# Optimization experiments

Measured on AMD Instinct MI355X. Metric: run time of the kernel, lower is better.

Reference implementation:

```python
import jax, jax.numpy as jnp
import numpy as np

N = 50000      # nodes
E = 800000     # edges (avg degree 16)
F_IN = 256     # input feature dim
D = 32         # per-head out dim (layer1)
H1 = 8         # layer1 heads
H2 = 1         # layer2 heads
C = 16         # num_classes


def setup_inputs() -> dict:
    key = jax.random.key(0)
    ks = jax.random.split(key, 11)
    s = 0.05  # weight scale
    return {
        "x": jax.random.normal(ks[0], (N, F_IN), dtype=jnp.float32),
        "src": jax.random.randint(ks[1], (E,), 0, N),
        "dst": jax.random.randint(ks[2], (E,), 0, N),
        "W1": jax.random.normal(ks[3], (F_IN, H1 * D), dtype=jnp.float32) * s,
        "al1": jax.random.normal(ks[4], (H1, D), dtype=jnp.float32) * s,
        "ar1": jax.random.normal(ks[5], (H1, D), dtype=jnp.float32) * s,
        "b1": jnp.zeros((H1 * D,), dtype=jnp.float32),
        "W2": jax.random.normal(ks[6], (H1 * D, H2 * C), dtype=jnp.float32) * s,
        "al2": jax.random.normal(ks[7], (H2, C), dtype=jnp.float32) * s,
        "ar2": jax.random.normal(ks[8], (H2, C), dtype=jnp.float32) * s,
        "b2": jnp.zeros((H2 * C,), dtype=jnp.float32),
    }


def gat_conv(src, dst, x, W, al, ar, b, neg_slope):
    """DGL-style GATConv (eval mode, no dropout, allow_zero_in_degree)."""
    n = x.shape[0]
    H, Dh = al.shape
    h = (x @ W).reshape(n, H, Dh)                      # [N,H,D]
    el = jnp.einsum('nhd,hd->nh', h, al)               # attn_l . h
    er = jnp.einsum('nhd,hd->nh', h, ar)               # attn_r . h
    e = el[src] + er[dst]                              # [E,H]
    e = jnp.where(e > 0, e, neg_slope * e)             # LeakyReLU
    # edge softmax over incoming edges of each dst node, per head
    m = jax.ops.segment_max(e, dst, num_segments=n)    # [N,H]
    m = jnp.where(jnp.isfinite(m), m, 0.0)             # empty segments -> 0
    ex = jnp.exp(e - m[dst])
    denom = jax.ops.segment_sum(ex, dst, num_segments=n)
    alpha = ex / denom[dst]                            # [E,H]
    # weighted scatter-add aggregation
    out = jax.ops.segment_sum(h[src] * alpha[:, :, None], dst, num_segments=n)
    return out + b.reshape(1, H, Dh)                   # [N,H,D]


def reference(x, src, dst, W1, al1, ar1, b1, W2, al2, ar2, b2):
    n = x.shape[0]
    x1 = gat_conv(src, dst, x, W1, al1, ar1, b1, 1.0).reshape(n, -1)  # flatten heads
    x1 = jax.nn.elu(x1)
    x2 = gat_conv(src, dst, x1, W2, al2, ar2, b2, 0.2)[:, 0, :]       # squeeze head dim
    return jax.nn.elu(x2)                                              # [N, C]
```

## Files before the change

kernel.cpp:

```cpp
#include <hip/hip_runtime.h>
#include <math.h>

typedef __attribute__((ext_vector_type(8))) short short8;
typedef __attribute__((ext_vector_type(4))) float f32x4;

__device__ __forceinline__ float elu_f(float v) {
    return v > 0.f ? v : __expf(v) - 1.f;
}

__device__ __forceinline__ unsigned short f2bf(float f) {
    unsigned u = __float_as_uint(f);
    unsigned r = (u + 0x7FFF + ((u >> 16) & 1)) >> 16;
    return (unsigned short)r;
}

__device__ __forceinline__ float bf2f(unsigned short u) {
    return __uint_as_float(((unsigned)u) << 16);
}

__global__ __launch_bounds__(256) void prep_kernel(const float* __restrict__ W1,
                                                   const float* __restrict__ al1, const float* __restrict__ ar1,
                                                   const float* __restrict__ W2,
                                                   const float* __restrict__ al2, const float* __restrict__ ar2,
                                                   unsigned short* __restrict__ W1t,
                                                   unsigned short* __restrict__ W2t) {
    int b = blockIdx.x, t = threadIdx.x;
    if (b < 256) {
        W1t[b * 256 + t] = f2bf(W1[t * 256 + b]);
    } else if (b == 256) {
        int k = t;
        #pragma unroll
        for (int h = 0; h < 8; h++) {
            float sl = 0.f, sr = 0.f;
            #pragma unroll
            for (int d = 0; d < 32; d++) {
                float wv = W1[k * 256 + 32 * h + d];
                sl += wv * al1[h * 32 + d];
                sr += wv * ar1[h * 32 + d];
            }
            W1t[(256 + h) * 256 + k] = f2bf(sl);
            W1t[(264 + h) * 256 + k] = f2bf(sr);
        }
    } else {
        int k = t;
        float sl = 0.f, sr = 0.f;
        #pragma unroll
        for (int c = 0; c < 16; c++) {
            float wv = W2[k * 16 + c];
            W2t[c * 256 + k] = f2bf(wv);
            sl += wv * al2[c];
            sr += wv * ar2[c];
        }
        W2t[16 * 256 + k] = f2bf(sl);
        W2t[17 * 256 + k] = f2bf(sr);
        #pragma unroll
        for (int c = 18; c < 32; c++) W2t[c * 256 + k] = 0;
    }
}

__global__ __launch_bounds__(256) void hist_kernel(const int* __restrict__ dst, int* __restrict__ cntmat,
                                                   int E, int nEB, int nbk) {
    __shared__ int hist[64];
    int b = blockIdx.x, t = threadIdx.x;
    if (t < nbk) hist[t] = 0;
    __syncthreads();
    int e0 = b * 2048 + t * 8;
    #pragma unroll
    for (int i = 0; i < 8; i += 4) {
        int e = e0 + i;
        if (e + 3 < E) {
            int4 d4 = *(const int4*)&dst[e];
            atomicAdd(&hist[d4.x >> 10], 1);
            atomicAdd(&hist[d4.y >> 10], 1);
            atomicAdd(&hist[d4.z >> 10], 1);
            atomicAdd(&hist[d4.w >> 10], 1);
        } else {
            for (int ee = e; ee < E && ee < e + 4; ee++) atomicAdd(&hist[dst[ee] >> 10], 1);
        }
    }
    __syncthreads();
    if (t < nbk) cntmat[t * nEB + b] = hist[t];
}

__global__ __launch_bounds__(256) void bsum_kernel(const int* __restrict__ cnt, int* __restrict__ bsum, int n) {
    int b = blockIdx.x, t = threadIdx.x;
    int i0 = b * 1024 + t * 4;
    int s = 0;
    #pragma unroll
    for (int k = 0; k < 4; k++) { int i = i0 + k; if (i < n) s += cnt[i]; }
    #pragma unroll
    for (int m = 1; m < 64; m <<= 1) s += __shfl_xor(s, m);
    __shared__ int ws[4];
    if ((t & 63) == 0) ws[t >> 6] = s;
    __syncthreads();
    if (t == 0) bsum[b] = ws[0] + ws[1] + ws[2] + ws[3];
}

__global__ __launch_bounds__(256) void scan_final_kernel(const int* __restrict__ cnt, const int* __restrict__ bsum,
                                                         int* __restrict__ offs, int n, int nb) {
    int b = blockIdx.x, t = threadIdx.x, lane = t & 63, w = t >> 6;
    __shared__ int ws[4];
    __shared__ int bbase_s;
    int i0 = b * 1024 + t * 4;
    int v[4]; int ts = 0;
    #pragma unroll
    for (int k = 0; k < 4; k++) { int i = i0 + k; v[k] = (i < n) ? cnt[i] : 0; ts += v[k]; }
    int x = ts;
    #pragma unroll
    for (int off = 1; off < 64; off <<= 1) {
        int y = __shfl_up(x, off);
        if (lane >= off) x += y;
    }
    if (lane == 63) ws[w] = x;
    if (w == 0) {
        int bv = (lane < nb) ? bsum[lane] : 0;
        int bx = bv;
        #pragma unroll
        for (int off = 1; off < 64; off <<= 1) {
            int y = __shfl_up(bx, off);
            if (lane >= off) bx += y;
        }
        if (lane == b) bbase_s = bx - bv;
    }
    __syncthreads();
    int wbase = 0;
    #pragma unroll
    for (int k = 0; k < 4; k++) if (k < w) wbase += ws[k];
    int base = bbase_s + wbase + (x - ts);
    #pragma unroll
    for (int k = 0; k < 4; k++) {
        int i = i0 + k;
        if (i < n) offs[i] = base;
        base += v[k];
        if (i == n - 1) offs[n] = base;
    }
}

__global__ __launch_bounds__(256) void bucket_scatter_kernel(const int* __restrict__ src,
                                                             const int* __restrict__ dst,
                                                             const int* __restrict__ scanned,
                                                             int2* __restrict__ ebuf,
                                                             int E, int nEB, int nbk) {
    __shared__ int sb[64];
    __shared__ int cur[64];
    int b = blockIdx.x, t = threadIdx.x;
    if (t < nbk) { sb[t] = scanned[t * nEB + b]; cur[t] = 0; }
    __syncthreads();
    int e0 = b * 2048 + t * 8;
    #pragma unroll
    for (int i = 0; i < 8; i += 4) {
        int e = e0 + i;
        if (e + 3 < E) {
            int4 d4 = *(const int4*)&dst[e];
            int4 s4 = *(const int4*)&src[e];
            int k, r;
            k = d4.x >> 10; r = atomicAdd(&cur[k], 1); ebuf[sb[k] + r] = make_int2(d4.x, s4.x);
            k = d4.y >> 10; r = atomicAdd(&cur[k], 1); ebuf[sb[k] + r] = make_int2(d4.y, s4.y);
            k = d4.z >> 10; r = atomicAdd(&cur[k], 1); ebuf[sb[k] + r] = make_int2(d4.z, s4.z);
            k = d4.w >> 10; r = atomicAdd(&cur[k], 1); ebuf[sb[k] + r] = make_int2(d4.w, s4.w);
        } else {
            for (int ee = e; ee < E && ee < e + 4; ee++) {
                int d = dst[ee];
                int k = d >> 10;
                int r = atomicAdd(&cur[k], 1);
                ebuf[sb[k] + r] = make_int2(d, src[ee]);
            }
        }
    }
}

__global__ __launch_bounds__(1024) void bucket_csr_kernel(const int2* __restrict__ ebuf,
                                                          const int* __restrict__ scanned,
                                                          int* __restrict__ offs, int* __restrict__ srt,
                                                          int N, int E, int nEB, int nbk) {
    __shared__ int lcnt[1024];
    __shared__ int lcur[1024];
    __shared__ int ws[16];
    int k = blockIdx.x, t = threadIdx.x;
    int lane = t & 63, w = t >> 6;
    int eb = scanned[k * nEB];
    int ee = (k + 1 < nbk) ? scanned[(k + 1) * nEB] : E;
    lcnt[t] = 0;
    __syncthreads();
    for (int e = eb + t; e < ee; e += 1024) {
        int2 p = ebuf[e];
        atomicAdd(&lcnt[p.x & 1023], 1);
    }
    __syncthreads();
    int v = lcnt[t];
    int x = v;
    #pragma unroll
    for (int off = 1; off < 64; off <<= 1) {
        int y = __shfl_up(x, off);
        if (lane >= off) x += y;
    }
    if (lane == 63) ws[w] = x;
    __syncthreads();
    if (w == 0) {
        int wv = (lane < 16) ? ws[lane] : 0;
        int wx = wv;
        #pragma unroll
        for (int off = 1; off < 16; off <<= 1) {
            int y = __shfl_up(wx, off);
            if (lane >= off) wx += y;
        }
        if (lane < 16) ws[lane] = wx - wv;
    }
    __syncthreads();
    int excl = ws[w] + (x - v);
    int node = (k << 10) + t;
    if (node < N) offs[node] = eb + excl;
    if (k == nbk - 1 && t == 0) offs[N] = E;
    lcur[t] = eb + excl;
    __syncthreads();
    for (int e = eb + t; e < ee; e += 1024) {
        int2 p = ebuf[e];
        int pos = atomicAdd(&lcur[p.x & 1023], 1);
        srt[pos] = p.y;
    }
}

#define STR1 40
__global__ __launch_bounds__(512) void gemm1_mfma(const float* __restrict__ x,
                                                  const unsigned short* __restrict__ W1t,
                                                  unsigned short* __restrict__ h,
                                                  float* __restrict__ el1, float* __restrict__ er1, int n) {
    __shared__ unsigned short As[128 * STR1];
    __shared__ unsigned short Bs[272 * STR1];
    int t = threadIdx.x;
    int w = t >> 6, l = t & 63;
    int rb = blockIdx.x * 128;
    f32x4 acc[17] = {};
    int ar = t >> 2;
    int ak = (t & 3) * 8;
    int lr = w * 16 + (l & 15);
    int lg = l >> 4;
    for (int kc = 0; kc < 256; kc += 32) {
        {
            int gr = rb + ar;
            float v[8];
            if (gr < n) {
                f32x4 v0 = *(const f32x4*)&x[(size_t)gr * 256 + kc + ak];
                f32x4 v1 = *(const f32x4*)&x[(size_t)gr * 256 + kc + ak + 4];
                v[0] = v0.x; v[1] = v0.y; v[2] = v0.z; v[3] = v0.w;
                v[4] = v1.x; v[5] = v1.y; v[6] = v1.z; v[7] = v1.w;
            } else {
                #pragma unroll
                for (int i = 0; i < 8; i++) v[i] = 0.f;
            }
            short8 bv;
            #pragma unroll
            for (int i = 0; i < 8; i++) bv[i] = (short)f2bf(v[i]);
            *(short8*)&As[ar * STR1 + ak] = bv;
        }
        #pragma unroll
        for (int i = 0; i < 3; i++) {
            int idx = t + i * 512;
            if (idx < 1088) {
                int bn = idx >> 2;
                int bk = (idx & 3) * 8;
                short8 bv = *(const short8*)&W1t[(size_t)bn * 256 + kc + bk];
                *(short8*)&Bs[bn * STR1 + bk] = bv;
            }
        }
        __syncthreads();
        short8 a = *(short8*)&As[lr * STR1 + lg * 8];
        #pragma unroll
        for (int j = 0; j < 17; j++) {
            short8 bfrag = *(short8*)&Bs[(j * 16 + (l & 15)) * STR1 + lg * 8];
            acc[j] = __builtin_amdgcn_mfma_f32_16x16x32_bf16(a, bfrag, acc[j], 0, 0, 0);
        }
        __syncthreads();
    }
    int r0 = rb + w * 16 + 4 * (l >> 4);
    int c0 = l & 15;
    #pragma unroll
    for (int j = 0; j < 16; j++) {
        #pragma unroll
        for (int i = 0; i < 4; i++) {
            int gr = r0 + i;
            if (gr < n) h[(size_t)gr * 256 + j * 16 + c0] = f2bf(acc[j][i]);
        }
    }
    #pragma unroll
    for (int i = 0; i < 4; i++) {
        int gr = r0 + i;
        if (gr < n) {
            if (c0 < 8) el1[gr * 8 + c0] = acc[16][i];
            else        er1[gr * 8 + (c0 - 8)] = acc[16][i];
        }
    }
}

__global__ __launch_bounds__(256) void agg1_kernel(const unsigned short* __restrict__ h1b,
                                                   const float* __restrict__ el1,
                                                   const float* __restrict__ er1, const float* __restrict__ b1,
                                                   const int* __restrict__ offs, const int* __restrict__ srt,
                                                   unsigned short* __restrict__ x1b, int n0, int n1) {
    int t = threadIdx.x; int lane = t & 63;
    int node = n0 + blockIdx.x * 4 + (t >> 6);
    if (node >= n1) return;
    int beg = offs[node], end = offs[node + 1];
    int q = lane & 31;
    int head = q >> 2;
    int half = lane >> 5;
    float er_h = er1[node * 8 + head];
    float acc[8] = {};
    float dsum = 0.f;
    for (int e = beg + half; e < end; e += 8) {
        int eB = e + 2, eC = e + 4, eD = e + 6;
        bool hB = eB < end, hC = eC < end, hD = eD < end;
        int sA = srt[e];
        int sB = srt[hB ? eB : e];
        int sC = srt[hC ? eC : e];
        int sD = srt[hD ? eD : e];
        float exA = __expf(el1[sA * 8 + head] + er_h);
        float exB = hB ? __expf(el1[sB * 8 + head] + er_h) : 0.f;
        float exC = hC ? __expf(el1[sC * 8 + head] + er_h) : 0.f;
        float exD = hD ? __expf(el1[sD * 8 + head] + er_h) : 0.f;
        short8 hA = *(const short8*)&h1b[(size_t)sA * 256 + q * 8];
        short8 hBv = *(const short8*)&h1b[(size_t)sB * 256 + q * 8];
        short8 hCv = *(const short8*)&h1b[(size_t)sC * 256 + q * 8];
        short8 hDv = *(const short8*)&h1b[(size_t)sD * 256 + q * 8];
        dsum += (exA + exB) + (exC + exD);
        #pragma unroll
        for (int k = 0; k < 8; k++)
            acc[k] += exA * bf2f((unsigned short)hA[k]) + exB * bf2f((unsigned short)hBv[k])
                    + exC * bf2f((unsigned short)hCv[k]) + exD * bf2f((unsigned short)hDv[k]);
    }
    dsum += __shfl_xor(dsum, 32);
    #pragma unroll
    for (int k = 0; k < 8; k++) acc[k] += __shfl_xor(acc[k], 32);
    if (half == 0) {
        float inv = dsum > 0.f ? 1.f / dsum : 0.f;
        f32x4 b0 = *(const f32x4*)&b1[q * 8];
        f32x4 b4 = *(const f32x4*)&b1[q * 8 + 4];
        float o[8];
        o[0] = elu_f(acc[0] * inv + b0.x); o[1] = elu_f(acc[1] * inv + b0.y);
        o[2] = elu_f(acc[2] * inv + b0.z); o[3] = elu_f(acc[3] * inv + b0.w);
        o[4] = elu_f(acc[4] * inv + b4.x); o[5] = elu_f(acc[5] * inv + b4.y);
        o[6] = elu_f(acc[6] * inv + b4.z); o[7] = elu_f(acc[7] * inv + b4.w);
        short8 ov;
        #pragma unroll
        for (int k = 0; k < 8; k++) ov[k] = (short)f2bf(o[k]);
        *(short8*)&x1b[(size_t)node * 256 + q * 8] = ov;
    }
}

__global__ __launch_bounds__(256) void gemm2_mfma(const unsigned short* __restrict__ x1b,
                                                  const unsigned short* __restrict__ W2t,
                                                  float* __restrict__ h2, float* __restrict__ el2,
                                                  float* __restrict__ er2, int n) {
    __shared__ unsigned short As[64 * STR1];
    __shared__ unsigned short Bs[32 * STR1];
    int t = threadIdx.x;
    int w = t >> 6, l = t & 63;
    int rb = blockIdx.x * 64;
    f32x4 acc[2] = {};
    int ar = t >> 2;
    int ak = (t & 3) * 8;
    int lr = w * 16 + (l & 15);
    int lg = l >> 4;
    for (int kc = 0; kc < 256; kc += 32) {
        {
            int gr = rb + ar;
            short8 av = {0, 0, 0, 0, 0, 0, 0, 0};
            if (gr < n) av = *(const short8*)&x1b[(size_t)gr * 256 + kc + ak];
            *(short8*)&As[ar * STR1 + ak] = av;
        }
        if (t < 128) {
            int bn = t >> 2, bk = (t & 3) * 8;
            short8 bv = *(const short8*)&W2t[(size_t)bn * 256 + kc + bk];
            *(short8*)&Bs[bn * STR1 + bk] = bv;
        }
        __syncthreads();
        short8 a = *(short8*)&As[lr * STR1 + lg * 8];
        #pragma unroll
        for (int j = 0; j < 2; j++) {
            short8 bfrag = *(short8*)&Bs[(j * 16 + (l & 15)) * STR1 + lg * 8];
            acc[j] = __builtin_amdgcn_mfma_f32_16x16x32_bf16(a, bfrag, acc[j], 0, 0, 0);
        }
        __syncthreads();
    }
    int r0 = rb + w * 16 + 4 * (l >> 4);
    int c0 = l & 15;
    #pragma unroll
    for (int i = 0; i < 4; i++) {
        int gr = r0 + i;
        if (gr < n) {
            h2[(size_t)gr * 16 + c0] = acc[0][i];
            if (c0 == 0) el2[gr] = acc[1][i];
            else if (c0 == 1) er2[gr] = acc[1][i];
        }
    }
}

__global__ __launch_bounds__(256) void agg2_kernel(const float* __restrict__ h2,
                                                   const float* __restrict__ el2,
                                                   const float* __restrict__ er2, const float* __restrict__ b2,
                                                   const int* __restrict__ offs, const int* __restrict__ srt,
                                                   float* __restrict__ out, int n) {
    int t = threadIdx.x; int lane = t & 63;
    int node = blockIdx.x * 4 + (t >> 6);
    if (node >= n) return;
    int beg = offs[node], end = offs[node + 1];
    int dim = lane & 15, eg = lane >> 4;
    float er_n = er2[node];
    float acc = 0.f, dsum = 0.f;
    for (int e = beg + eg; e < end; e += 16) {
        int eB = e + 4, eC = e + 8, eD = e + 12;
        bool hB = eB < end, hC = eC < end, hD = eD < end;
        int sA = srt[e];
        int sB = srt[hB ? eB : e];
        int sC = srt[hC ? eC : e];
        int sD = srt[hD ? eD : e];
        float evA = el2[sA] + er_n; evA = fmaxf(evA, 0.2f * evA);
        float evB = el2[sB] + er_n; evB = fmaxf(evB, 0.2f * evB);
        float evC = el2[sC] + er_n; evC = fmaxf(evC, 0.2f * evC);
        float evD = el2[sD] + er_n; evD = fmaxf(evD, 0.2f * evD);
        float exA = __expf(evA);
        float exB = hB ? __expf(evB) : 0.f;
        float exC = hC ? __expf(evC) : 0.f;
        float exD = hD ? __expf(evD) : 0.f;
        float hA = h2[(size_t)sA * 16 + dim];
        float hBv = h2[(size_t)sB * 16 + dim];
        float hCv = h2[(size_t)sC * 16 + dim];
        float hDv = h2[(size_t)sD * 16 + dim];
        dsum += (exA + exB) + (exC + exD);
        acc += exA * hA + exB * hBv + exC * hCv + exD * hDv;
    }
    acc += __shfl_xor(acc, 16); acc += __shfl_xor(acc, 32);
    dsum += __shfl_xor(dsum, 16); dsum += __shfl_xor(dsum, 32);
    float inv = dsum > 0.f ? 1.f / dsum : 0.f;
    float o = elu_f(acc * inv + b2[dim]);
    if (lane < 16) out[(size_t)node * 16 + dim] = o;
}

extern "C" void kernel_launch(void* const* d_in, const int* in_sizes, int n_in,
                              void* d_out, int out_size, void* d_ws, size_t ws_size,
                              hipStream_t stream) {
    const float* x   = (const float*)d_in[0];
    const int*   src = (const int*)d_in[1];
    const int*   dst = (const int*)d_in[2];
    const float* W1  = (const float*)d_in[3];
    const float* al1 = (const float*)d_in[4];
    const float* ar1 = (const float*)d_in[5];
    const float* b1  = (const float*)d_in[6];
    const float* W2  = (const float*)d_in[7];
    const float* al2 = (const float*)d_in[8];
    const float* ar2 = (const float*)d_in[9];
    const float* b2  = (const float*)d_in[10];
    const int N = in_sizes[0] / 256;
    const int E = in_sizes[1];

    char* wsp = (char*)d_ws;
    size_t off = 0;
    auto alloc = [&](size_t bytes) -> void* {
        void* p = wsp + off;
        off = (off + bytes + 255) & ~(size_t)255;
        return p;
    };
    unsigned short* h1b = (unsigned short*)alloc((size_t)N * 256 * 2);
    unsigned short* x1b = (unsigned short*)alloc((size_t)N * 256 * 2);
    float* el1 = (float*)alloc((size_t)N * 8 * 4);
    float* er1 = (float*)alloc((size_t)N * 8 * 4);
    float* h2  = (float*)alloc((size_t)N * 16 * 4);
    float* el2 = (float*)alloc((size_t)N * 4);
    float* er2 = (float*)alloc((size_t)N * 4);
    int*   offs = (int*)alloc((size_t)(N + 1) * 4);
    int*   srt  = (int*)alloc((size_t)E * 4);
    int2*  ebuf = (int2*)alloc((size_t)E * 8);
    unsigned short* W1t = (unsigned short*)alloc((size_t)272 * 256 * 2);
    unsigned short* W2t = (unsigned short*)alloc((size_t)32 * 256 * 2);

    const int nEB = (E + 2047) / 2048;
    const int nbk = (N + 1023) >> 10;
    const int n2  = nbk * nEB;
    const int NB2 = (n2 + 1023) / 1024;

    int* cntmat  = (int*)alloc((size_t)n2 * 4);
    int* scanned = (int*)alloc((size_t)(n2 + 1) * 4);
    int* bsum    = (int*)alloc((size_t)64 * 4);

    prep_kernel<<<258, 256, 0, stream>>>(W1, al1, ar1, W2, al2, ar2, W1t, W2t);
    hist_kernel<<<nEB, 256, 0, stream>>>(dst, cntmat, E, nEB, nbk);
    bsum_kernel<<<NB2, 256, 0, stream>>>(cntmat, bsum, n2);
    scan_final_kernel<<<NB2, 256, 0, stream>>>(cntmat, bsum, scanned, n2, NB2);
    bucket_scatter_kernel<<<nEB, 256, 0, stream>>>(src, dst, scanned, ebuf, E, nEB, nbk);
    bucket_csr_kernel<<<nbk, 1024, 0, stream>>>(ebuf, scanned, offs, srt, N, E, nEB, nbk);

    gemm1_mfma<<<(N + 127) / 128, 512, 0, stream>>>(x, W1t, h1b, el1, er1, N);
    const int Nh = N / 2;
    agg1_kernel<<<(Nh + 3) / 4, 256, 0, stream>>>(h1b, el1, er1, b1, offs, srt, x1b, 0, Nh);
    agg1_kernel<<<(N - Nh + 3) / 4, 256, 0, stream>>>(h1b, el1, er1, b1, offs, srt, x1b, Nh, N);
    gemm2_mfma<<<(N + 63) / 64, 256, 0, stream>>>(x1b, W2t, h2, el2, er2, N);
    agg2_kernel<<<(N + 3) / 4, 256, 0, stream>>>(h2, el2, er2, b2, offs, srt, (float*)d_out, N);
}
```

Before: 168.6 us.

## Fuse layer-2 projection into layer-1 aggregation kernel, drop x1 buffer

The layer-1 aggregation kernel now applies ELU and immediately multiplies each node's 256-wide hidden vector by W2 (plus the folded attention vectors) using per-lane dot products and wavefront shuffle reductions. It writes h2, el2 and er2 directly, which removes the bf16 x1 intermediate, its round trip through global memory, and the separate MFMA GEMM2 launch. The cost is extra scalar FMAs and shuffle reductions in the memory-bound aggregation kernel. The kernel is also launched once instead of twice.

```diff
diff --git a/kernel.cpp b/kernel.cpp
--- a/kernel.cpp
+++ b/kernel.cpp
@@ -53,8 +53,6 @@
         }
         W2t[16 * 256 + k] = f2bf(sl);
         W2t[17 * 256 + k] = f2bf(sr);
-        #pragma unroll
-        for (int c = 18; c < 32; c++) W2t[c * 256 + k] = 0;
     }
 }
 
@@ -292,14 +290,17 @@
     }
 }
 
-__global__ __launch_bounds__(256) void agg1_kernel(const unsigned short* __restrict__ h1b,
-                                                   const float* __restrict__ el1,
-                                                   const float* __restrict__ er1, const float* __restrict__ b1,
-                                                   const int* __restrict__ offs, const int* __restrict__ srt,
-                                                   unsigned short* __restrict__ x1b, int n0, int n1) {
+__global__ __launch_bounds__(256) void agg1_fused_kernel(const unsigned short* __restrict__ h1b,
+                                                         const float* __restrict__ el1,
+                                                         const float* __restrict__ er1,
+                                                         const float* __restrict__ b1,
+                                                         const unsigned short* __restrict__ W2t,
+                                                         const int* __restrict__ offs, const int* __restrict__ srt,
+                                                         float* __restrict__ h2, float* __restrict__ el2,
+                                                         float* __restrict__ er2, int n) {
     int t = threadIdx.x; int lane = t & 63;
-    int node = n0 + blockIdx.x * 4 + (t >> 6);
-    if (node >= n1) return;
+    int node = blockIdx.x * 4 + (t >> 6);
+    if (node >= n) return;
     int beg = offs[node], end = offs[node + 1];
     int q = lane & 31;
     int head = q >> 2;
@@ -331,67 +332,38 @@
     dsum += __shfl_xor(dsum, 32);
     #pragma unroll
     for (int k = 0; k < 8; k++) acc[k] += __shfl_xor(acc[k], 32);
+    float inv = dsum > 0.f ? 1.f / dsum : 0.f;
+    f32x4 b0 = *(const f32x4*)&b1[q * 8];
+    f32x4 b4 = *(const f32x4*)&b1[q * 8 + 4];
+    float o[8];
+    o[0] = elu_f(acc[0] * inv + b0.x); o[1] = elu_f(acc[1] * inv + b0.y);
+    o[2] = elu_f(acc[2] * inv + b0.z); o[3] = elu_f(acc[3] * inv + b0.w);
+    o[4] = elu_f(acc[4] * inv + b4.x); o[5] = elu_f(acc[5] * inv + b4.y);
+    o[6] = elu_f(acc[6] * inv + b4.z); o[7] = elu_f(acc[7] * inv + b4.w);
+    float outv = 0.f;
+    #pragma unroll
+    for (int g = 0; g < 3; g++) {
+        float part[6];
+        #pragma unroll
+        for (int c = 0; c < 6; c++) {
+            short8 wv = *(const short8*)&W2t[(g * 6 + c) * 256 + q * 8];
+            float s = 0.f;
+            #pragma unroll
+            for (int j = 0; j < 8; j++) s += o[j] * bf2f((unsigned short)wv[j]);
+            part[c] = s;
+        }
+        #pragma unroll
+        for (int mask = 1; mask < 32; mask <<= 1) {
+            #pragma unroll
+            for (int c = 0; c < 6; c++) part[c] += __shfl_xor(part[c], mask);
+        }
+        #pragma unroll
+        for (int c = 0; c < 6; c++) if (q == g * 6 + c) outv = part[c];
+    }
     if (half == 0) {
-        float inv = dsum > 0.f ? 1.f / dsum : 0.f;
-        f32x4 b0 = *(const f32x4*)&b1[q * 8];
-        f32x4 b4 = *(const f32x4*)&b1[q * 8 + 4];
-        float o[8];
-        o[0] = elu_f(acc[0] * inv + b0.x); o[1] = elu_f(acc[1] * inv + b0.y);
-        o[2] = elu_f(acc[2] * inv + b0.z); o[3] = elu_f(acc[3] * inv + b0.w);
-        o[4] = elu_f(acc[4] * inv + b4.x); o[5] = elu_f(acc[5] * inv + b4.y);
-        o[6] = elu_f(acc[6] * inv + b4.z); o[7] = elu_f(acc[7] * inv + b4.w);
-        short8 ov;
-        #pragma unroll
-        for (int k = 0; k < 8; k++) ov[k] = (short)f2bf(o[k]);
-        *(short8*)&x1b[(size_t)node * 256 + q * 8] = ov;
-    }
-}
-
-__global__ __launch_bounds__(256) void gemm2_mfma(const unsigned short* __restrict__ x1b,
-                                                  const unsigned short* __restrict__ W2t,
-                                                  float* __restrict__ h2, float* __restrict__ el2,
-                                                  float* __restrict__ er2, int n) {
-    __shared__ unsigned short As[64 * STR1];
-    __shared__ unsigned short Bs[32 * STR1];
-    int t = threadIdx.x;
-    int w = t >> 6, l = t & 63;
-    int rb = blockIdx.x * 64;
-    f32x4 acc[2] = {};
-    int ar = t >> 2;
-    int ak = (t & 3) * 8;
-    int lr = w * 16 + (l & 15);
-    int lg = l >> 4;
-    for (int kc = 0; kc < 256; kc += 32) {
-        {
-            int gr = rb + ar;
-            short8 av = {0, 0, 0, 0, 0, 0, 0, 0};
-            if (gr < n) av = *(const short8*)&x1b[(size_t)gr * 256 + kc + ak];
-            *(short8*)&As[ar * STR1 + ak] = av;
-        }
-        if (t < 128) {
-            int bn = t >> 2, bk = (t & 3) * 8;
-            short8 bv = *(const short8*)&W2t[(size_t)bn * 256 + kc + bk];
-            *(short8*)&Bs[bn * STR1 + bk] = bv;
-        }
-        __syncthreads();
-        short8 a = *(short8*)&As[lr * STR1 + lg * 8];
-        #pragma unroll
-        for (int j = 0; j < 2; j++) {
-            short8 bfrag = *(short8*)&Bs[(j * 16 + (l & 15)) * STR1 + lg * 8];
-            acc[j] = __builtin_amdgcn_mfma_f32_16x16x32_bf16(a, bfrag, acc[j], 0, 0, 0);
-        }
-        __syncthreads();
-    }
-    int r0 = rb + w * 16 + 4 * (l >> 4);
-    int c0 = l & 15;
-    #pragma unroll
-    for (int i = 0; i < 4; i++) {
-        int gr = r0 + i;
-        if (gr < n) {
-            h2[(size_t)gr * 16 + c0] = acc[0][i];
-            if (c0 == 0) el2[gr] = acc[1][i];
-            else if (c0 == 1) er2[gr] = acc[1][i];
-        }
+        if (q < 16) h2[(size_t)node * 16 + q] = outv;
+        else if (q == 16) el2[node] = outv;
+        else if (q == 17) er2[node] = outv;
     }
 }
 
@@ -461,7 +433,6 @@
         return p;
     };
     unsigned short* h1b = (unsigned short*)alloc((size_t)N * 256 * 2);
-    unsigned short* x1b = (unsigned short*)alloc((size_t)N * 256 * 2);
     float* el1 = (float*)alloc((size_t)N * 8 * 4);
     float* er1 = (float*)alloc((size_t)N * 8 * 4);
     float* h2  = (float*)alloc((size_t)N * 16 * 4);
@@ -471,7 +442,7 @@
     int*   srt  = (int*)alloc((size_t)E * 4);
     int2*  ebuf = (int2*)alloc((size_t)E * 8);
     unsigned short* W1t = (unsigned short*)alloc((size_t)272 * 256 * 2);
-    unsigned short* W2t = (unsigned short*)alloc((size_t)32 * 256 * 2);
+    unsigned short* W2t = (unsigned short*)alloc((size_t)18 * 256 * 2);
 
     const int nEB = (E + 2047) / 2048;
     const int nbk = (N + 1023) >> 10;
@@ -490,9 +461,7 @@
     bucket_csr_kernel<<<nbk, 1024, 0, stream>>>(ebuf, scanned, offs, srt, N, E, nEB, nbk);
 
     gemm1_mfma<<<(N + 127) / 128, 512, 0, stream>>>(x, W1t, h1b, el1, er1, N);
-    const int Nh = N / 2;
-    agg1_kernel<<<(Nh + 3) / 4, 256, 0, stream>>>(h1b, el1, er1, b1, offs, srt, x1b, 0, Nh);
-    agg1_kernel<<<(N - Nh + 3) / 4, 256, 0, stream>>>(h1b, el1, er1, b1, offs, srt, x1b, Nh, N);
-    gemm2_mfma<<<(N + 63) / 64, 256, 0, stream>>>(x1b, W2t, h2, el2, er2, N);
+    agg1_fused_kernel<<<(N + 3) / 4, 256, 0, stream>>>(h1b, el1, er1, b1, W2t, offs, srt,
+                                                       h2, el2, er2, N);
     agg2_kernel<<<(N + 3) / 4, 256, 0, stream>>>(h2, el2, er2, b2, offs, srt, (float*)d_out, N);
 }
```

New measurement: 174.0 us. +3.2%, slower.

## Fuse weight prep with histogram and bucket scatter with layer-1 GEMM

Applied to the files above, without the earlier changes.

Merges the weight-prep kernel into the histogram kernel, and the bucket-scatter kernel into the layer-1 MFMA GEMM as one heterogeneous launch whose blocks alternate between scatter and GEMM roles. The two half-range agg1 launches are also collapsed into one. The goal is to cut launch count and let the independent CSR-build work overlap with the GEMM on idle CUs. In exchange, scatter blocks now run with 512 threads and carry the GEMM's large shared-memory allocation, which can lower occupancy.

```diff
diff --git a/kernel.cpp b/kernel.cpp
--- a/kernel.cpp
+++ b/kernel.cpp
@@ -18,16 +18,41 @@
     return __uint_as_float(((unsigned)u) << 16);
 }
 
-__global__ __launch_bounds__(256) void prep_kernel(const float* __restrict__ W1,
-                                                   const float* __restrict__ al1, const float* __restrict__ ar1,
-                                                   const float* __restrict__ W2,
-                                                   const float* __restrict__ al2, const float* __restrict__ ar2,
-                                                   unsigned short* __restrict__ W1t,
-                                                   unsigned short* __restrict__ W2t) {
+__global__ __launch_bounds__(256) void prep_hist_kernel(const int* __restrict__ dst, int* __restrict__ cntmat,
+                                                        int E, int nEB, int nbk,
+                                                        const float* __restrict__ W1,
+                                                        const float* __restrict__ al1, const float* __restrict__ ar1,
+                                                        const float* __restrict__ W2,
+                                                        const float* __restrict__ al2, const float* __restrict__ ar2,
+                                                        unsigned short* __restrict__ W1t,
+                                                        unsigned short* __restrict__ W2t) {
+    __shared__ int hist[64];
     int b = blockIdx.x, t = threadIdx.x;
-    if (b < 256) {
-        W1t[b * 256 + t] = f2bf(W1[t * 256 + b]);
-    } else if (b == 256) {
+    if (b < nEB) {
+        if (t < nbk) hist[t] = 0;
+        __syncthreads();
+        int e0 = b * 2048 + t * 8;
+        #pragma unroll
+        for (int i = 0; i < 8; i += 4) {
+            int e = e0 + i;
+            if (e + 3 < E) {
+                int4 d4 = *(const int4*)&dst[e];
+                atomicAdd(&hist[d4.x >> 10], 1);
+                atomicAdd(&hist[d4.y >> 10], 1);
+                atomicAdd(&hist[d4.z >> 10], 1);
+                atomicAdd(&hist[d4.w >> 10], 1);
+            } else {
+                for (int ee = e; ee < E && ee < e + 4; ee++) atomicAdd(&hist[dst[ee] >> 10], 1);
+            }
+        }
+        __syncthreads();
+        if (t < nbk) cntmat[t * nEB + b] = hist[t];
+        return;
+    }
+    int bb = b - nEB;
+    if (bb < 256) {
+        W1t[bb * 256 + t] = f2bf(W1[t * 256 + bb]);
+    } else if (bb == 256) {
         int k = t;
         #pragma unroll
         for (int h = 0; h < 8; h++) {
@@ -58,30 +83,6 @@
     }
 }
 
-__global__ __launch_bounds__(256) void hist_kernel(const int* __restrict__ dst, int* __restrict__ cntmat,
-                                                   int E, int nEB, int nbk) {
-    __shared__ int hist[64];
-    int b = blockIdx.x, t = threadIdx.x;
-    if (t < nbk) hist[t] = 0;
-    __syncthreads();
-    int e0 = b * 2048 + t * 8;
-    #pragma unroll
-    for (int i = 0; i < 8; i += 4) {
-        int e = e0 + i;
-        if (e + 3 < E) {
-            int4 d4 = *(const int4*)&dst[e];
-            atomicAdd(&hist[d4.x >> 10], 1);
-            atomicAdd(&hist[d4.y >> 10], 1);
-            atomicAdd(&hist[d4.z >> 10], 1);
-            atomicAdd(&hist[d4.w >> 10], 1);
-        } else {
-            for (int ee = e; ee < E && ee < e + 4; ee++) atomicAdd(&hist[dst[ee] >> 10], 1);
-        }
-    }
-    __syncthreads();
-    if (t < nbk) cntmat[t * nEB + b] = hist[t];
-}
-
 __global__ __launch_bounds__(256) void bsum_kernel(const int* __restrict__ cnt, int* __restrict__ bsum, int n) {
     int b = blockIdx.x, t = threadIdx.x;
     int i0 = b * 1024 + t * 4;
@@ -136,100 +137,54 @@
     }
 }
 
-__global__ __launch_bounds__(256) void bucket_scatter_kernel(const int* __restrict__ src,
-                                                             const int* __restrict__ dst,
-                                                             const int* __restrict__ scanned,
-                                                             int2* __restrict__ ebuf,
-                                                             int E, int nEB, int nbk) {
+#define STR1 40
+__global__ __launch_bounds__(512) void scatter_gemm1_kernel(const int* __restrict__ src,
+                                                            const int* __restrict__ dst,
+                                                            const int* __restrict__ scanned,
+                                                            int2* __restrict__ ebuf,
+                                                            int E, int nEB, int nbk,
+                                                            const float* __restrict__ x,
+                                                            const unsigned short* __restrict__ W1t,
+                                                            unsigned short* __restrict__ h,
+                                                            float* __restrict__ el1, float* __restrict__ er1,
+                                                            int n, int nGB) {
+    __shared__ unsigned short As[128 * STR1];
+    __shared__ unsigned short Bs[272 * STR1];
     __shared__ int sb[64];
     __shared__ int cur[64];
     int b = blockIdx.x, t = threadIdx.x;
-    if (t < nbk) { sb[t] = scanned[t * nEB + b]; cur[t] = 0; }
-    __syncthreads();
-    int e0 = b * 2048 + t * 8;
-    #pragma unroll
-    for (int i = 0; i < 8; i += 4) {
-        int e = e0 + i;
-        if (e + 3 < E) {
-            int4 d4 = *(const int4*)&dst[e];
-            int4 s4 = *(const int4*)&src[e];
+    int nPair = (nEB < nGB) ? nEB : nGB;
+    int type, id;
+    if (b < 2 * nPair) { type = b & 1; id = b >> 1; }
+    else {
+        int r = b - 2 * nPair;
+        if (nEB > nGB) { type = 0; id = nPair + r; }
+        else           { type = 1; id = nPair + r; }
+    }
+    if (type == 0) {
+        if (t < nbk) { sb[t] = scanned[t * nEB + id]; cur[t] = 0; }
+        __syncthreads();
+        int e0 = id * 2048 + t * 4;
+        if (e0 + 3 < E) {
+            int4 d4 = *(const int4*)&dst[e0];
+            int4 s4 = *(const int4*)&src[e0];
             int k, r;
             k = d4.x >> 10; r = atomicAdd(&cur[k], 1); ebuf[sb[k] + r] = make_int2(d4.x, s4.x);
             k = d4.y >> 10; r = atomicAdd(&cur[k], 1); ebuf[sb[k] + r] = make_int2(d4.y, s4.y);
             k = d4.z >> 10; r = atomicAdd(&cur[k], 1); ebuf[sb[k] + r] = make_int2(d4.z, s4.z);
             k = d4.w >> 10; r = atomicAdd(&cur[k], 1); ebuf[sb[k] + r] = make_int2(d4.w, s4.w);
         } else {
-            for (int ee = e; ee < E && ee < e + 4; ee++) {
+            for (int ee = e0; ee < E && ee < e0 + 4; ee++) {
                 int d = dst[ee];
                 int k = d >> 10;
                 int r = atomicAdd(&cur[k], 1);
                 ebuf[sb[k] + r] = make_int2(d, src[ee]);
             }
         }
-    }
-}
-
-__global__ __launch_bounds__(1024) void bucket_csr_kernel(const int2* __restrict__ ebuf,
-                                                          const int* __restrict__ scanned,
-                                                          int* __restrict__ offs, int* __restrict__ srt,
-                                                          int N, int E, int nEB, int nbk) {
-    __shared__ int lcnt[1024];
-    __shared__ int lcur[1024];
-    __shared__ int ws[16];
-    int k = blockIdx.x, t = threadIdx.x;
-    int lane = t & 63, w = t >> 6;
-    int eb = scanned[k * nEB];
-    int ee = (k + 1 < nbk) ? scanned[(k + 1) * nEB] : E;
-    lcnt[t] = 0;
-    __syncthreads();
-    for (int e = eb + t; e < ee; e += 1024) {
-        int2 p = ebuf[e];
-        atomicAdd(&lcnt[p.x & 1023], 1);
-    }
-    __syncthreads();
-    int v = lcnt[t];
-    int x = v;
-    #pragma unroll
-    for (int off = 1; off < 64; off <<= 1) {
-        int y = __shfl_up(x, off);
-        if (lane >= off) x += y;
-    }
-    if (lane == 63) ws[w] = x;
-    __syncthreads();
-    if (w == 0) {
-        int wv = (lane < 16) ? ws[lane] : 0;
-        int wx = wv;
-        #pragma unroll
-        for (int off = 1; off < 16; off <<= 1) {
-            int y = __shfl_up(wx, off);
-            if (lane >= off) wx += y;
-        }
-        if (lane < 16) ws[lane] = wx - wv;
-    }
-    __syncthreads();
-    int excl = ws[w] + (x - v);
-    int node = (k << 10) + t;
-    if (node < N) offs[node] = eb + excl;
-    if (k == nbk - 1 && t == 0) offs[N] = E;
-    lcur[t] = eb + excl;
-    __syncthreads();
-    for (int e = eb + t; e < ee; e += 1024) {
-        int2 p = ebuf[e];
-        int pos = atomicAdd(&lcur[p.x & 1023], 1);
-        srt[pos] = p.y;
-    }
-}
-
-#define STR1 40
-__global__ __launch_bounds__(512) void gemm1_mfma(const float* __restrict__ x,
-                                                  const unsigned short* __restrict__ W1t,
-                                                  unsigned short* __restrict__ h,
-                                                  float* __restrict__ el1, float* __restrict__ er1, int n) {
-    __shared__ unsigned short As[128 * STR1];
-    __shared__ unsigned short Bs[272 * STR1];
-    int t = threadIdx.x;
+        return;
+    }
     int w = t >> 6, l = t & 63;
-    int rb = blockIdx.x * 128;
+    int rb = id * 128;
     f32x4 acc[17] = {};
     int ar = t >> 2;
     int ak = (t & 3) * 8;
@@ -292,14 +247,65 @@
     }
 }
 
+__global__ __launch_bounds__(1024) void bucket_csr_kernel(const int2* __restrict__ ebuf,
+                                                          const int* __restrict__ scanned,
+                                                          int* __restrict__ offs, int* __restrict__ srt,
+                                                          int N, int E, int nEB, int nbk) {
+    __shared__ int lcnt[1024];
+    __shared__ int lcur[1024];
+    __shared__ int ws[16];
+    int k = blockIdx.x, t = threadIdx.x;
+    int lane = t & 63, w = t >> 6;
+    int eb = scanned[k * nEB];
+    int ee = (k + 1 < nbk) ? scanned[(k + 1) * nEB] : E;
+    lcnt[t] = 0;
+    __syncthreads();
+    for (int e = eb + t; e < ee; e += 1024) {
+        int2 p = ebuf[e];
+        atomicAdd(&lcnt[p.x & 1023], 1);
+    }
+    __syncthreads();
+    int v = lcnt[t];
+    int x = v;
+    #pragma unroll
+    for (int off = 1; off < 64; off <<= 1) {
+        int y = __shfl_up(x, off);
+        if (lane >= off) x += y;
+    }
+    if (lane == 63) ws[w] = x;
+    __syncthreads();
+    if (w == 0) {
+        int wv = (lane < 16) ? ws[lane] : 0;
+        int wx = wv;
+        #pragma unroll
+        for (int off = 1; off < 16; off <<= 1) {
+            int y = __shfl_up(wx, off);
+            if (lane >= off) wx += y;
+        }
+        if (lane < 16) ws[lane] = wx - wv;
+    }
+    __syncthreads();
+    int excl = ws[w] + (x - v);
+    int node = (k << 10) + t;
+    if (node < N) offs[node] = eb + excl;
+    if (k == nbk - 1 && t == 0) offs[N] = E;
+    lcur[t] = eb + excl;
+    __syncthreads();
+    for (int e = eb + t; e < ee; e += 1024) {
+        int2 p = ebuf[e];
+        int pos = atomicAdd(&lcur[p.x & 1023], 1);
+        srt[pos] = p.y;
+    }
+}
+
 __global__ __launch_bounds__(256) void agg1_kernel(const unsigned short* __restrict__ h1b,
                                                    const float* __restrict__ el1,
                                                    const float* __restrict__ er1, const float* __restrict__ b1,
                                                    const int* __restrict__ offs, const int* __restrict__ srt,
-                                                   unsigned short* __restrict__ x1b, int n0, int n1) {
+                                                   unsigned short* __restrict__ x1b, int n) {
     int t = threadIdx.x; int lane = t & 63;
-    int node = n0 + blockIdx.x * 4 + (t >> 6);
-    if (node >= n1) return;
+    int node = blockIdx.x * 4 + (t >> 6);
+    if (node >= n) return;
     int beg = offs[node], end = offs[node + 1];
     int q = lane & 31;
     int head = q >> 2;
@@ -477,22 +483,21 @@
     const int nbk = (N + 1023) >> 10;
     const int n2  = nbk * nEB;
     const int NB2 = (n2 + 1023) / 1024;
+    const int nGB = (N + 127) / 128;
 
     int* cntmat  = (int*)alloc((size_t)n2 * 4);
     int* scanned = (int*)alloc((size_t)(n2 + 1) * 4);
     int* bsum    = (int*)alloc((size_t)64 * 4);
 
-    prep_kernel<<<258, 256, 0, stream>>>(W1, al1, ar1, W2, al2, ar2, W1t, W2t);
-    hist_kernel<<<nEB, 256, 0, stream>>>(dst, cntmat, E, nEB, nbk);
+    prep_hist_kernel<<<nEB + 258, 256, 0, stream>>>(dst, cntmat, E, nEB, nbk,
+                                                    W1, al1, ar1, W2, al2, ar2, W1t, W2t);
     bsum_kernel<<<NB2, 256, 0, stream>>>(cntmat, bsum, n2);
     scan_final_kernel<<<NB2, 256, 0, stream>>>(cntmat, bsum, scanned, n2, NB2);
-    bucket_scatter_kernel<<<nEB, 256, 0, stream>>>(src, dst, scanned, ebuf, E, nEB, nbk);
+    scatter_gemm1_kernel<<<nEB + nGB, 512, 0, stream>>>(src, dst, scanned, ebuf, E, nEB, nbk,
+                                                        x, W1t, h1b, el1, er1, N, nGB);
     bucket_csr_kernel<<<nbk, 1024, 0, stream>>>(ebuf, scanned, offs, srt, N, E, nEB, nbk);
 
-    gemm1_mfma<<<(N + 127) / 128, 512, 0, stream>>>(x, W1t, h1b, el1, er1, N);
-    const int Nh = N / 2;
-    agg1_kernel<<<(Nh + 3) / 4, 256, 0, stream>>>(h1b, el1, er1, b1, offs, srt, x1b, 0, Nh);
-    agg1_kernel<<<(N - Nh + 3) / 4, 256, 0, stream>>>(h1b, el1, er1, b1, offs, srt, x1b, Nh, N);
+    agg1_kernel<<<(N + 3) / 4, 256, 0, stream>>>(h1b, el1, er1, b1, offs, srt, x1b, N);
     gemm2_mfma<<<(N + 63) / 64, 256, 0, stream>>>(x1b, W2t, h2, el2, er2, N);
     agg2_kernel<<<(N + 3) / 4, 256, 0, stream>>>(h2, el2, er2, b2, offs, srt, (float*)d_out, N);
 }
```

Result: slower. 174.0 us (+3.2%).
